# Kernel optimization log

Hardware: AMD Instinct MI355X
Metric: run time of the kernel (lower is better)

## Reference

```python
import jax, jax.numpy as jnp
import numpy as np

IN_DIM = 1024
OUT_DIM = 1024
NUM_EXPERTS = 8
TOP_K = 2
B = 8192


def setup_inputs() -> dict:
    key = jax.random.key(0)
    ks = jax.random.split(key, 8)
    s_in = 1.0 / np.sqrt(IN_DIM)
    s_out = 1.0 / np.sqrt(OUT_DIM)
    return {
        "x": jax.random.normal(ks[0], (B, IN_DIM), dtype=jnp.float32),
        # router Linear(in_dim, num_experts)
        "rw": jax.random.uniform(ks[1], (IN_DIM, NUM_EXPERTS), jnp.float32, -s_in, s_in),
        "rb": jax.random.uniform(ks[2], (NUM_EXPERTS,), jnp.float32, -s_in, s_in),
        # expert MLPs stacked along expert axis
        "w1": jax.random.uniform(ks[3], (NUM_EXPERTS, IN_DIM, OUT_DIM), jnp.float32, -s_in, s_in),
        "b1": jax.random.uniform(ks[4], (NUM_EXPERTS, OUT_DIM), jnp.float32, -s_in, s_in),
        "w2": jax.random.uniform(ks[5], (NUM_EXPERTS, OUT_DIM, OUT_DIM), jnp.float32, -s_out, s_out),
        "b2": jax.random.uniform(ks[6], (NUM_EXPERTS, OUT_DIM), jnp.float32, -s_out, s_out),
    }


def reference(x, rw, rb, w1, b1, w2, b2):
    # ---- TopkRouter ----
    logits = x @ rw + rb                                  # [B, E]
    topk_vals, topk_idx = jax.lax.top_k(logits, TOP_K)    # [B, K]
    neg_inf = jnp.full_like(logits, -jnp.inf)
    rows = jnp.arange(logits.shape[0])[:, None]
    sparse_logits = neg_inf.at[rows, topk_idx].set(topk_vals)
    gating = jax.nn.softmax(sparse_logits, axis=-1)       # zeros outside top-k

    # ---- experts: dense compute, gating weights are exactly 0 for
    # non-selected experts so the weighted combine matches the masked
    # dispatch of the original module. ----
    h = jax.nn.relu(jnp.einsum('bi,eio->beo', x, w1) + b1[None])   # [B, E, out]
    y = jnp.einsum('beh,eho->beo', h, w2) + b2[None]               # [B, E, out]
    fused = jnp.einsum('beo,be->bo', y, gating)                    # [B, out]
    return fused, gating
```

## Files before the change

### kernel.cpp

```cpp
#include <hip/hip_runtime.h>
#include <hip/hip_bf16.h>
#include <cstdint>
#include <cstddef>

#define IN_DIM 1024
#define OUT_DIM 1024
#define NE 8
#define NTOK 8192
#define MT_TILES 20

typedef __bf16 bf16x8 __attribute__((ext_vector_type(8)));
typedef float f32x4 __attribute__((ext_vector_type(4)));
typedef unsigned short ushort8v __attribute__((ext_vector_type(8)));

__device__ __forceinline__ unsigned short f2bf(float f) {
    unsigned u = __float_as_uint(f);
    unsigned r = 0x7fffu + ((u >> 16) & 1u);
    return (unsigned short)((u + r) >> 16);
}

__device__ __forceinline__ void bf2x(unsigned u, float& lo, float& hi) {
    lo = __uint_as_float(u << 16);
    hi = __uint_as_float(u & 0xffff0000u);
}

__device__ __forceinline__ void async16(void* lds, const void* g) {
    __builtin_amdgcn_global_load_lds(
        (const __attribute__((address_space(1))) unsigned int*)g,
        (__attribute__((address_space(3))) unsigned int*)lds,
        16, 0, 0);
}

__global__ __launch_bounds__(256) void convert_transpose_kernel(
    const float* __restrict__ w1, const float* __restrict__ w2,
    unsigned short* __restrict__ w1T, unsigned short* __restrict__ w2T) {
    __shared__ float tile[64][68];
    int z = blockIdx.z;
    const float* src = (z < 8) ? (w1 + (size_t)z * IN_DIM * OUT_DIM)
                               : (w2 + (size_t)(z - 8) * OUT_DIM * OUT_DIM);
    unsigned short* dst = (z < 8) ? (w1T + (size_t)z * IN_DIM * OUT_DIM)
                                  : (w2T + (size_t)(z - 8) * OUT_DIM * OUT_DIM);
    int kt = blockIdx.x * 64, nt = blockIdx.y * 64;
    int t = threadIdx.x;
    int r = t >> 2, cq = (t & 3) * 16;
#pragma unroll
    for (int q = 0; q < 4; ++q) {
        float4 v = *(const float4*)(src + (size_t)(kt + r) * 1024 + nt + cq + q * 4);
        tile[r][cq + q * 4 + 0] = v.x;
        tile[r][cq + q * 4 + 1] = v.y;
        tile[r][cq + q * 4 + 2] = v.z;
        tile[r][cq + q * 4 + 3] = v.w;
    }
    __syncthreads();
    int n = t >> 2, kq = (t & 3) * 16;
#pragma unroll
    for (int q = 0; q < 2; ++q) {
        ushort8v o;
#pragma unroll
        for (int i = 0; i < 8; ++i) o[i] = f2bf(tile[kq + q * 8 + i][n]);
        *(ushort8v*)(dst + (size_t)(nt + n) * 1024 + kt + kq + q * 8) = o;
    }
}

__global__ __launch_bounds__(256) void router_kernel(
    const float* __restrict__ x, const float* __restrict__ rw,
    const float* __restrict__ rb,
    unsigned short* __restrict__ xb,
    float* __restrict__ gating, int* __restrict__ enc,
    float2* __restrict__ gw, int* __restrict__ cnt) {
    __shared__ float srw[NE * IN_DIM];
    int t = threadIdx.x;
    if (blockIdx.x == 0 && t < NE) cnt[t] = 0;
#pragma unroll
    for (int i = 0; i < 4; ++i) {
        int k = t + i * 256;
        float4 a = *(const float4*)(rw + (size_t)k * NE);
        float4 b = *(const float4*)(rw + (size_t)k * NE + 4);
        srw[0 * IN_DIM + k] = a.x; srw[1 * IN_DIM + k] = a.y;
        srw[2 * IN_DIM + k] = a.z; srw[3 * IN_DIM + k] = a.w;
        srw[4 * IN_DIM + k] = b.x; srw[5 * IN_DIM + k] = b.y;
        srw[6 * IN_DIM + k] = b.z; srw[7 * IN_DIM + k] = b.w;
    }
    __syncthreads();
    int wave = t >> 6, lane = t & 63;
    int tok = blockIdx.x * 4 + wave;
    const float* xrow = x + (size_t)tok * IN_DIM;
    unsigned short* xbrow = xb + (size_t)tok * IN_DIM;
    float acc[NE] = {0, 0, 0, 0, 0, 0, 0, 0};
#pragma unroll
    for (int i = 0; i < 4; ++i) {
        int k = i * 256 + lane * 4;
        float4 xv = *(const float4*)(xrow + k);
        ushort4 o;
        o.x = f2bf(xv.x); o.y = f2bf(xv.y); o.z = f2bf(xv.z); o.w = f2bf(xv.w);
        *(ushort4*)(xbrow + k) = o;
#pragma unroll
        for (int e = 0; e < NE; ++e) {
            float4 wv = *(const float4*)(srw + e * IN_DIM + k);
            acc[e] = fmaf(xv.x, wv.x, fmaf(xv.y, wv.y, fmaf(xv.z, wv.z, fmaf(xv.w, wv.w, acc[e]))));
        }
    }
#pragma unroll
    for (int e = 0; e < NE; ++e) {
#pragma unroll
        for (int off = 32; off > 0; off >>= 1) acc[e] += __shfl_xor(acc[e], off);
        acc[e] += rb[e];
    }
    int e0 = 0; float v0 = acc[0];
#pragma unroll
    for (int e = 1; e < NE; ++e) if (acc[e] > v0) { v0 = acc[e]; e0 = e; }
    int e1 = -1; float v1 = -3.4e38f;
#pragma unroll
    for (int e = 0; e < NE; ++e) if (e != e0 && acc[e] > v1) { v1 = acc[e]; e1 = e; }
    float tg = __expf(v1 - v0);
    float inv = 1.0f / (1.0f + tg);
    float g0 = inv, g1 = tg * inv;
    if (lane < NE) gating[(size_t)tok * NE + lane] = (lane == e0) ? g0 : ((lane == e1) ? g1 : 0.0f);
    if (lane == 0) {
        enc[tok] = e0 | (e1 << 8);
        gw[tok] = make_float2(g0, g1);
    }
}

__global__ __launch_bounds__(256) void bucket_kernel(
    const int* __restrict__ enc,
    int* __restrict__ bidx, int* __restrict__ slots, int* __restrict__ cnt) {
    int tok = blockIdx.x * 256 + threadIdx.x;
    int lane = threadIdx.x & 63;
    int v = enc[tok];
    int e0 = v & 0xff, e1 = (v >> 8) & 0xff;
    unsigned long long below = (1ull << lane) - 1ull;
    int p0 = 0, p1 = 0;
#pragma unroll
    for (int e = 0; e < NE; ++e) {
        unsigned long long m0 = __ballot(e0 == e);
        unsigned long long m1 = __ballot(e1 == e);
        int c0 = __popcll(m0), c1 = __popcll(m1);
        int base = 0;
        if (lane == 0 && (c0 + c1)) base = atomicAdd(&cnt[e], c0 + c1);
        base = __shfl(base, 0);
        if (e0 == e) p0 = base + __popcll(m0 & below);
        if (e1 == e) p1 = base + c0 + __popcll(m1 & below);
    }
    bidx[e0 * NTOK + p0] = tok;
    bidx[e1 * NTOK + p1] = tok;
    slots[2 * tok + 0] = (e0 << 13) | p0;
    slots[2 * tok + 1] = (e1 << 13) | p1;
}

__device__ __forceinline__ int prefix_cnt(const int* __restrict__ cnt, int e) {
    int s = 0;
    for (int i = 0; i < NE; ++i) s += (i < e) ? cnt[i] : 0;
    return s;
}

__device__ __forceinline__ void kstep(const unsigned short* Ab,
                                      const unsigned short* Bb,
                                      f32x4 (&acc)[4][4], int wm, int wn,
                                      int lhalf, int slot) {
    bf16x8 av[4], bv[4];
#pragma unroll
    for (int i = 0; i < 4; ++i)
        av[i] = *(const bf16x8*)(Ab + (wm * 32 + i * 8 + lhalf) * 64 + slot);
#pragma unroll
    for (int j = 0; j < 4; ++j)
        bv[j] = *(const bf16x8*)(Bb + (wn * 32 + j * 8 + lhalf) * 64 + slot);
#pragma unroll
    for (int i = 0; i < 4; ++i)
#pragma unroll
        for (int j = 0; j < 4; ++j)
            acc[i][j] = __builtin_amdgcn_mfma_f32_16x16x32_bf16(av[i], bv[j], acc[i][j], 0, 0, 0);
}


__global__ __launch_bounds__(256) void gemm1_kernel(
    const unsigned short* __restrict__ xb, const unsigned short* __restrict__ w1T,
    const float* __restrict__ b1, const int* __restrict__ bidx,
    const int* __restrict__ cnt,
    unsigned short* __restrict__ H) {
    int b = blockIdx.x;
    int e = b & 7;
    int t2 = b >> 3;
    int nt = t2 & 7;
    int mt = t2 >> 3;
    int n_e = cnt[e];
    if (mt * 128 >= n_e) return;
    __shared__ __attribute__((aligned(16))) unsigned short As[3][64 * 64];
    __shared__ __attribute__((aligned(16))) unsigned short Bs[3][64 * 64];
    int t = threadIdx.x, wave = t >> 6, lane = t & 63;
    const int* be = bidx + e * NTOK;
    const unsigned short* agp[2]; const unsigned short* bgp[2];
    int ldsoff[2];
#pragma unroll
    for (int is = 0; is < 2; ++is) {
        int c = is * 256 + t;
        int line = c >> 3;
        int chunkg = (c & 7) ^ (line & 7);
        int sub = chunkg >> 2;
        int growl = 2 * line + sub;
        int growlB = (line >> 5) * 64 + (line & 7) * 8 + sub * 4 + ((line >> 3) & 3);
        int gcol = (chunkg & 3) * 8;
        int gra = mt * 128 + growl;
        int grac = gra < n_e ? gra : n_e - 1;
        agp[is] = xb + (size_t)be[grac] * IN_DIM + gcol;
        bgp[is] = w1T + ((size_t)e * OUT_DIM + nt * 128 + growlB) * IN_DIM + gcol;
        ldsoff[is] = (is * 256 + wave * 64) * 8;
    }
    int wm = wave & 1, wn = wave >> 1;
    int quad = lane >> 4, l15 = lane & 15;
    int lhalf = l15 >> 1;
    int slot = (((l15 & 1) * 4 + quad) ^ lhalf) * 8;
    f32x4 zero4 = {0.f, 0.f, 0.f, 0.f};
    f32x4 acc[4][4];
#pragma unroll
    for (int i = 0; i < 4; ++i)
#pragma unroll
        for (int j = 0; j < 4; ++j) acc[i][j] = zero4;

#pragma unroll
    for (int pt = 0; pt < 2; ++pt)
#pragma unroll
        for (int is = 0; is < 2; ++is) {
            async16(&As[pt][ldsoff[is]], agp[is] + pt * 32);
            async16(&Bs[pt][ldsoff[is]], bgp[is] + pt * 32);
        }
    int cb = 0, sb = 2;
    for (int it = 0; it < 31; ++it) {
        asm volatile("s_waitcnt vmcnt(4)\n\ts_barrier" ::: "memory");
        if (it < 30) {
            int ktn = (it + 2) * 32;
#pragma unroll
            for (int is = 0; is < 2; ++is) {
                async16(&As[sb][ldsoff[is]], agp[is] + ktn);
                async16(&Bs[sb][ldsoff[is]], bgp[is] + ktn);
            }
        }
        kstep(As[cb], Bs[cb], acc, wm, wn, lhalf, slot);
        cb = (cb == 2) ? 0 : cb + 1;
        sb = (sb == 2) ? 0 : sb + 1;
    }
    asm volatile("s_waitcnt vmcnt(0)\n\ts_barrier" ::: "memory");
    kstep(As[cb], Bs[cb], acc, wm, wn, lhalf, slot);

    int hbase = prefix_cnt(cnt, e);
    const float* b1e = b1 + (size_t)e * OUT_DIM;
    int n0 = nt * 128 + wn * 64 + l15 * 4;
    float4 bias = *(const float4*)(b1e + n0);
#pragma unroll
    for (int i = 0; i < 4; ++i) {
        int m0 = mt * 128 + wm * 64 + i * 16 + quad * 4;
#pragma unroll
        for (int r = 0; r < 4; ++r) {
            int gm = m0 + r;
            if (gm < n_e) {
                float h0 = acc[i][0][r] + bias.x; h0 = h0 > 0.f ? h0 : 0.f;
                float h1 = acc[i][1][r] + bias.y; h1 = h1 > 0.f ? h1 : 0.f;
                float h2 = acc[i][2][r] + bias.z; h2 = h2 > 0.f ? h2 : 0.f;
                float h3 = acc[i][3][r] + bias.w; h3 = h3 > 0.f ? h3 : 0.f;
                ushort4 o;
                o.x = f2bf(h0); o.y = f2bf(h1); o.z = f2bf(h2); o.w = f2bf(h3);
                *(ushort4*)(H + (size_t)(hbase + gm) * OUT_DIM + n0) = o;
            }
        }
    }
}

__global__ __launch_bounds__(256) void gemm2_kernel(
    const unsigned short* __restrict__ H, const unsigned short* __restrict__ w2T,
    const int* __restrict__ cnt,
    unsigned short* __restrict__ Y) {
    int b = blockIdx.x;
    int e = b & 7;
    int t2 = b >> 3;
    int nt = t2 & 7;
    int mt = t2 >> 3;
    int n_e = cnt[e];
    if (mt * 128 >= n_e) return;
    __shared__ __attribute__((aligned(16))) unsigned short As[3][64 * 64];
    __shared__ __attribute__((aligned(16))) unsigned short Bs[3][64 * 64];
    int t = threadIdx.x, wave = t >> 6, lane = t & 63;
    int hbase = prefix_cnt(cnt, e);
    const unsigned short* agp[2]; const unsigned short* bgp[2];
    int ldsoff[2];
#pragma unroll
    for (int is = 0; is < 2; ++is) {
        int c = is * 256 + t;
        int line = c >> 3;
        int chunkg = (c & 7) ^ (line & 7);
        int sub = chunkg >> 2;
        int growl = 2 * line + sub;
        int growlB = (line >> 5) * 64 + (line & 7) * 8 + sub * 4 + ((line >> 3) & 3);
        int gcol = (chunkg & 3) * 8;
        int gra = mt * 128 + growl;
        int grac = gra < n_e ? gra : n_e - 1;
        agp[is] = H + (size_t)(hbase + grac) * OUT_DIM + gcol;
        bgp[is] = w2T + ((size_t)e * OUT_DIM + nt * 128 + growlB) * OUT_DIM + gcol;
        ldsoff[is] = (is * 256 + wave * 64) * 8;
    }
    int wm = wave & 1, wn = wave >> 1;
    int quad = lane >> 4, l15 = lane & 15;
    int lhalf = l15 >> 1;
    int slot = (((l15 & 1) * 4 + quad) ^ lhalf) * 8;
    f32x4 zero4 = {0.f, 0.f, 0.f, 0.f};
    f32x4 acc[4][4];
#pragma unroll
    for (int i = 0; i < 4; ++i)
#pragma unroll
        for (int j = 0; j < 4; ++j) acc[i][j] = zero4;

#pragma unroll
    for (int pt = 0; pt < 2; ++pt)
#pragma unroll
        for (int is = 0; is < 2; ++is) {
            async16(&As[pt][ldsoff[is]], agp[is] + pt * 32);
            async16(&Bs[pt][ldsoff[is]], bgp[is] + pt * 32);
        }
    int cb = 0, sb = 2;
    for (int it = 0; it < 31; ++it) {
        asm volatile("s_waitcnt vmcnt(4)\n\ts_barrier" ::: "memory");
        if (it < 30) {
            int ktn = (it + 2) * 32;
#pragma unroll
            for (int is = 0; is < 2; ++is) {
                async16(&As[sb][ldsoff[is]], agp[is] + ktn);
                async16(&Bs[sb][ldsoff[is]], bgp[is] + ktn);
            }
        }
        kstep(As[cb], Bs[cb], acc, wm, wn, lhalf, slot);
        cb = (cb == 2) ? 0 : cb + 1;
        sb = (sb == 2) ? 0 : sb + 1;
    }
    asm volatile("s_waitcnt vmcnt(0)\n\ts_barrier" ::: "memory");
    kstep(As[cb], Bs[cb], acc, wm, wn, lhalf, slot);

    int n0 = nt * 128 + wn * 64 + l15 * 4;
#pragma unroll
    for (int i = 0; i < 4; ++i) {
        int m0 = mt * 128 + wm * 64 + i * 16 + quad * 4;
#pragma unroll
        for (int r = 0; r < 4; ++r) {
            int gm = m0 + r;
            if (gm < n_e) {
                ushort4 o;
                o.x = f2bf(acc[i][0][r]); o.y = f2bf(acc[i][1][r]);
                o.z = f2bf(acc[i][2][r]); o.w = f2bf(acc[i][3][r]);
                *(ushort4*)(Y + (size_t)(hbase + gm) * OUT_DIM + n0) = o;
            }
        }
    }
}

__global__ __launch_bounds__(256) void combine_kernel(
    const unsigned short* __restrict__ Y, const float* __restrict__ b2,
    const float2* __restrict__ gw, const int* __restrict__ slots,
    const int* __restrict__ cnt, float* __restrict__ out) {
    int t = threadIdx.x, wave = t >> 6, lane = t & 63;
    int tok = blockIdx.x * 4 + wave;
    int pre[NE];
    {
        int s = 0;
#pragma unroll
        for (int i = 0; i < NE; ++i) { pre[i] = s; s += cnt[i]; }
    }
    int s0 = slots[2 * tok], s1 = slots[2 * tok + 1];
    int e0 = s0 >> 13, e1 = s1 >> 13;
    int r0 = pre[e0] + (s0 & 8191);
    int r1 = pre[e1] + (s1 & 8191);
    float2 g = gw[tok];
    const unsigned short* y0 = Y + (size_t)r0 * OUT_DIM;
    const unsigned short* y1 = Y + (size_t)r1 * OUT_DIM;
    const float* c0 = b2 + (size_t)e0 * OUT_DIM;
    const float* c1 = b2 + (size_t)e1 * OUT_DIM;
    float* orow = out + (size_t)tok * OUT_DIM;
#pragma unroll
    for (int i = 0; i < 2; ++i) {
        int c = i * 512 + lane * 8;
        uint4 ua = *(const uint4*)(y0 + c);
        uint4 ub = *(const uint4*)(y1 + c);
        float a[8], b[8];
        bf2x(ua.x, a[0], a[1]); bf2x(ua.y, a[2], a[3]);
        bf2x(ua.z, a[4], a[5]); bf2x(ua.w, a[6], a[7]);
        bf2x(ub.x, b[0], b[1]); bf2x(ub.y, b[2], b[3]);
        bf2x(ub.z, b[4], b[5]); bf2x(ub.w, b[6], b[7]);
        float4 p0 = *(const float4*)(c0 + c);
        float4 p1 = *(const float4*)(c0 + c + 4);
        float4 q0 = *(const float4*)(c1 + c);
        float4 q1 = *(const float4*)(c1 + c + 4);
        float o[8];
        o[0] = g.x * (a[0] + p0.x) + g.y * (b[0] + q0.x);
        o[1] = g.x * (a[1] + p0.y) + g.y * (b[1] + q0.y);
        o[2] = g.x * (a[2] + p0.z) + g.y * (b[2] + q0.z);
        o[3] = g.x * (a[3] + p0.w) + g.y * (b[3] + q0.w);
        o[4] = g.x * (a[4] + p1.x) + g.y * (b[4] + q1.x);
        o[5] = g.x * (a[5] + p1.y) + g.y * (b[5] + q1.y);
        o[6] = g.x * (a[6] + p1.z) + g.y * (b[6] + q1.z);
        o[7] = g.x * (a[7] + p1.w) + g.y * (b[7] + q1.w);
        *(float4*)(orow + c) = make_float4(o[0], o[1], o[2], o[3]);
        *(float4*)(orow + c + 4) = make_float4(o[4], o[5], o[6], o[7]);
    }
}

extern "C" void kernel_launch(void* const* d_in, const int* in_sizes, int n_in,
                              void* d_out, int out_size, void* d_ws, size_t ws_size,
                              hipStream_t stream) {
    const float* x  = (const float*)d_in[0];
    const float* rw = (const float*)d_in[1];
    const float* rb = (const float*)d_in[2];
    const float* w1 = (const float*)d_in[3];
    const float* b1 = (const float*)d_in[4];
    const float* w2 = (const float*)d_in[5];
    const float* b2 = (const float*)d_in[6];
    float* out = (float*)d_out;
    float* gating = out + (size_t)NTOK * OUT_DIM;

    char* ws = (char*)d_ws;
    unsigned short* xb  = (unsigned short*)(ws + 0);
    unsigned short* Y   = (unsigned short*)(ws + 0);
    unsigned short* w1T = (unsigned short*)(ws + 16777216);
    unsigned short* w2T = (unsigned short*)(ws + 33554432);
    unsigned short* H   = (unsigned short*)(ws + 50331648);
    int*   bidx  = (int*)(ws + 83886080);
    int*   slots = (int*)(ws + 84148224);
    int*   cnt   = (int*)(ws + 84213760);
    int*    enc  = (int*)(ws + 84213888);
    float2* gw   = (float2*)(ws + 84246656);

    convert_transpose_kernel<<<dim3(16, 16, 16), 256, 0, stream>>>(w1, w2, w1T, w2T);
    router_kernel<<<NTOK / 4, 256, 0, stream>>>(x, rw, rb, xb, gating, enc, gw, cnt);
    bucket_kernel<<<NTOK / 256, 256, 0, stream>>>(enc, bidx, slots, cnt);
    gemm1_kernel<<<8 * 8 * MT_TILES, 256, 0, stream>>>(xb, w1T, b1, bidx, cnt, H);
    gemm2_kernel<<<8 * 8 * MT_TILES, 256, 0, stream>>>(H, w2T, cnt, Y);
    combine_kernel<<<NTOK / 4, 256, 0, stream>>>(Y, b2, gw, slots, cnt, out);
    (void)in_sizes; (void)n_in; (void)out_size; (void)ws_size;
}
```

Before: 294.7 us.

## Enlarge expert GEMM M-tile to 256 rows with 8x4 MFMA accumulators per wave

Doubles the token (M) tile of both expert GEMMs from 128 to 256 rows, so each wave computes 8x4 MFMA blocks instead of 4x4. Each B (weight) tile loaded into LDS is now reused across twice as many rows, cutting weight traffic and halving the grid. The cost is larger A buffers in LDS (triple-buffered), more accumulator registers with a launch-bounds occupancy hint of 2, and coarser tiles that waste more work on ragged per-expert token counts.

```diff
diff --git a/kernel.cpp b/kernel.cpp
--- a/kernel.cpp
+++ b/kernel.cpp
@@ -7,7 +7,7 @@
 #define OUT_DIM 1024
 #define NE 8
 #define NTOK 8192
-#define MT_TILES 20
+#define MT_TILES 10
 
 typedef __bf16 bf16x8 __attribute__((ext_vector_type(8)));
 typedef float f32x4 __attribute__((ext_vector_type(4)));
@@ -156,24 +156,24 @@
 
 __device__ __forceinline__ void kstep(const unsigned short* Ab,
                                       const unsigned short* Bb,
-                                      f32x4 (&acc)[4][4], int wm, int wn,
+                                      f32x4 (&acc)[8][4], int wm, int wn,
                                       int lhalf, int slot) {
-    bf16x8 av[4], bv[4];
-#pragma unroll
-    for (int i = 0; i < 4; ++i)
-        av[i] = *(const bf16x8*)(Ab + (wm * 32 + i * 8 + lhalf) * 64 + slot);
+    bf16x8 av[8], bv[4];
+#pragma unroll
+    for (int i = 0; i < 8; ++i)
+        av[i] = *(const bf16x8*)(Ab + (wm * 64 + i * 8 + lhalf) * 64 + slot);
 #pragma unroll
     for (int j = 0; j < 4; ++j)
         bv[j] = *(const bf16x8*)(Bb + (wn * 32 + j * 8 + lhalf) * 64 + slot);
 #pragma unroll
-    for (int i = 0; i < 4; ++i)
+    for (int i = 0; i < 8; ++i)
 #pragma unroll
         for (int j = 0; j < 4; ++j)
             acc[i][j] = __builtin_amdgcn_mfma_f32_16x16x32_bf16(av[i], bv[j], acc[i][j], 0, 0, 0);
 }
 
 
-__global__ __launch_bounds__(256) void gemm1_kernel(
+__global__ __launch_bounds__(256, 2) void gemm1_kernel(
     const unsigned short* __restrict__ xb, const unsigned short* __restrict__ w1T,
     const float* __restrict__ b1, const int* __restrict__ bidx,
     const int* __restrict__ cnt,
@@ -184,56 +184,64 @@
     int nt = t2 & 7;
     int mt = t2 >> 3;
     int n_e = cnt[e];
-    if (mt * 128 >= n_e) return;
-    __shared__ __attribute__((aligned(16))) unsigned short As[3][64 * 64];
+    if (mt * 256 >= n_e) return;
+    __shared__ __attribute__((aligned(16))) unsigned short As[3][128 * 64];
     __shared__ __attribute__((aligned(16))) unsigned short Bs[3][64 * 64];
     int t = threadIdx.x, wave = t >> 6, lane = t & 63;
     const int* be = bidx + e * NTOK;
-    const unsigned short* agp[2]; const unsigned short* bgp[2];
-    int ldsoff[2];
+    const unsigned short* agp[4]; const unsigned short* bgp[2];
+    int ldsoffA[4], ldsoffB[2];
+#pragma unroll
+    for (int is = 0; is < 4; ++is) {
+        int c = is * 256 + t;
+        int line = c >> 3;
+        int chunkg = (c & 7) ^ (line & 7);
+        int sub = chunkg >> 2;
+        int growl = 2 * line + sub;
+        int gcol = (chunkg & 3) * 8;
+        int gra = mt * 256 + growl;
+        int grac = gra < n_e ? gra : n_e - 1;
+        agp[is] = xb + (size_t)be[grac] * IN_DIM + gcol;
+        ldsoffA[is] = (is * 256 + wave * 64) * 8;
+    }
 #pragma unroll
     for (int is = 0; is < 2; ++is) {
         int c = is * 256 + t;
         int line = c >> 3;
         int chunkg = (c & 7) ^ (line & 7);
         int sub = chunkg >> 2;
-        int growl = 2 * line + sub;
         int growlB = (line >> 5) * 64 + (line & 7) * 8 + sub * 4 + ((line >> 3) & 3);
         int gcol = (chunkg & 3) * 8;
-        int gra = mt * 128 + growl;
-        int grac = gra < n_e ? gra : n_e - 1;
-        agp[is] = xb + (size_t)be[grac] * IN_DIM + gcol;
         bgp[is] = w1T + ((size_t)e * OUT_DIM + nt * 128 + growlB) * IN_DIM + gcol;
-        ldsoff[is] = (is * 256 + wave * 64) * 8;
+        ldsoffB[is] = (is * 256 + wave * 64) * 8;
     }
     int wm = wave & 1, wn = wave >> 1;
     int quad = lane >> 4, l15 = lane & 15;
     int lhalf = l15 >> 1;
     int slot = (((l15 & 1) * 4 + quad) ^ lhalf) * 8;
     f32x4 zero4 = {0.f, 0.f, 0.f, 0.f};
-    f32x4 acc[4][4];
-#pragma unroll
-    for (int i = 0; i < 4; ++i)
+    f32x4 acc[8][4];
+#pragma unroll
+    for (int i = 0; i < 8; ++i)
 #pragma unroll
         for (int j = 0; j < 4; ++j) acc[i][j] = zero4;
 
 #pragma unroll
-    for (int pt = 0; pt < 2; ++pt)
-#pragma unroll
-        for (int is = 0; is < 2; ++is) {
-            async16(&As[pt][ldsoff[is]], agp[is] + pt * 32);
-            async16(&Bs[pt][ldsoff[is]], bgp[is] + pt * 32);
-        }
+    for (int pt = 0; pt < 2; ++pt) {
+#pragma unroll
+        for (int is = 0; is < 4; ++is) async16(&As[pt][ldsoffA[is]], agp[is] + pt * 32);
+#pragma unroll
+        for (int is = 0; is < 2; ++is) async16(&Bs[pt][ldsoffB[is]], bgp[is] + pt * 32);
+    }
     int cb = 0, sb = 2;
     for (int it = 0; it < 31; ++it) {
-        asm volatile("s_waitcnt vmcnt(4)\n\ts_barrier" ::: "memory");
+        asm volatile("s_waitcnt vmcnt(6)\n\ts_barrier" ::: "memory");
         if (it < 30) {
             int ktn = (it + 2) * 32;
 #pragma unroll
-            for (int is = 0; is < 2; ++is) {
-                async16(&As[sb][ldsoff[is]], agp[is] + ktn);
-                async16(&Bs[sb][ldsoff[is]], bgp[is] + ktn);
-            }
+            for (int is = 0; is < 4; ++is) async16(&As[sb][ldsoffA[is]], agp[is] + ktn);
+#pragma unroll
+            for (int is = 0; is < 2; ++is) async16(&Bs[sb][ldsoffB[is]], bgp[is] + ktn);
         }
         kstep(As[cb], Bs[cb], acc, wm, wn, lhalf, slot);
         cb = (cb == 2) ? 0 : cb + 1;
@@ -247,8 +255,8 @@
     int n0 = nt * 128 + wn * 64 + l15 * 4;
     float4 bias = *(const float4*)(b1e + n0);
 #pragma unroll
-    for (int i = 0; i < 4; ++i) {
-        int m0 = mt * 128 + wm * 64 + i * 16 + quad * 4;
+    for (int i = 0; i < 8; ++i) {
+        int m0 = mt * 256 + wm * 128 + i * 16 + quad * 4;
 #pragma unroll
         for (int r = 0; r < 4; ++r) {
             int gm = m0 + r;
@@ -265,7 +273,7 @@
     }
 }
 
-__global__ __launch_bounds__(256) void gemm2_kernel(
+__global__ __launch_bounds__(256, 2) void gemm2_kernel(
     const unsigned short* __restrict__ H, const unsigned short* __restrict__ w2T,
     const int* __restrict__ cnt,
     unsigned short* __restrict__ Y) {
@@ -275,56 +283,64 @@
     int nt = t2 & 7;
     int mt = t2 >> 3;
     int n_e = cnt[e];
-    if (mt * 128 >= n_e) return;
-    __shared__ __attribute__((aligned(16))) unsigned short As[3][64 * 64];
+    if (mt * 256 >= n_e) return;
+    __shared__ __attribute__((aligned(16))) unsigned short As[3][128 * 64];
     __shared__ __attribute__((aligned(16))) unsigned short Bs[3][64 * 64];
     int t = threadIdx.x, wave = t >> 6, lane = t & 63;
     int hbase = prefix_cnt(cnt, e);
-    const unsigned short* agp[2]; const unsigned short* bgp[2];
-    int ldsoff[2];
+    const unsigned short* agp[4]; const unsigned short* bgp[2];
+    int ldsoffA[4], ldsoffB[2];
+#pragma unroll
+    for (int is = 0; is < 4; ++is) {
+        int c = is * 256 + t;
+        int line = c >> 3;
+        int chunkg = (c & 7) ^ (line & 7);
+        int sub = chunkg >> 2;
+        int growl = 2 * line + sub;
+        int gcol = (chunkg & 3) * 8;
+        int gra = mt * 256 + growl;
+        int grac = gra < n_e ? gra : n_e - 1;
+        agp[is] = H + (size_t)(hbase + grac) * OUT_DIM + gcol;
+        ldsoffA[is] = (is * 256 + wave * 64) * 8;
+    }
 #pragma unroll
     for (int is = 0; is < 2; ++is) {
         int c = is * 256 + t;
         int line = c >> 3;
         int chunkg = (c & 7) ^ (line & 7);
         int sub = chunkg >> 2;
-        int growl = 2 * line + sub;
         int growlB = (line >> 5) * 64 + (line & 7) * 8 + sub * 4 + ((line >> 3) & 3);
         int gcol = (chunkg & 3) * 8;
-        int gra = mt * 128 + growl;
-        int grac = gra < n_e ? gra : n_e - 1;
-        agp[is] = H + (size_t)(hbase + grac) * OUT_DIM + gcol;
         bgp[is] = w2T + ((size_t)e * OUT_DIM + nt * 128 + growlB) * OUT_DIM + gcol;
-        ldsoff[is] = (is * 256 + wave * 64) * 8;
+        ldsoffB[is] = (is * 256 + wave * 64) * 8;
     }
     int wm = wave & 1, wn = wave >> 1;
     int quad = lane >> 4, l15 = lane & 15;
     int lhalf = l15 >> 1;
     int slot = (((l15 & 1) * 4 + quad) ^ lhalf) * 8;
     f32x4 zero4 = {0.f, 0.f, 0.f, 0.f};
-    f32x4 acc[4][4];
-#pragma unroll
-    for (int i = 0; i < 4; ++i)
+    f32x4 acc[8][4];
+#pragma unroll
+    for (int i = 0; i < 8; ++i)
 #pragma unroll
         for (int j = 0; j < 4; ++j) acc[i][j] = zero4;
 
 #pragma unroll
-    for (int pt = 0; pt < 2; ++pt)
-#pragma unroll
-        for (int is = 0; is < 2; ++is) {
-            async16(&As[pt][ldsoff[is]], agp[is] + pt * 32);
-            async16(&Bs[pt][ldsoff[is]], bgp[is] + pt * 32);
-        }
+    for (int pt = 0; pt < 2; ++pt) {
+#pragma unroll
+        for (int is = 0; is < 4; ++is) async16(&As[pt][ldsoffA[is]], agp[is] + pt * 32);
+#pragma unroll
+        for (int is = 0; is < 2; ++is) async16(&Bs[pt][ldsoffB[is]], bgp[is] + pt * 32);
+    }
     int cb = 0, sb = 2;
     for (int it = 0; it < 31; ++it) {
-        asm volatile("s_waitcnt vmcnt(4)\n\ts_barrier" ::: "memory");
+        asm volatile("s_waitcnt vmcnt(6)\n\ts_barrier" ::: "memory");
         if (it < 30) {
             int ktn = (it + 2) * 32;
 #pragma unroll
-            for (int is = 0; is < 2; ++is) {
-                async16(&As[sb][ldsoff[is]], agp[is] + ktn);
-                async16(&Bs[sb][ldsoff[is]], bgp[is] + ktn);
-            }
+            for (int is = 0; is < 4; ++is) async16(&As[sb][ldsoffA[is]], agp[is] + ktn);
+#pragma unroll
+            for (int is = 0; is < 2; ++is) async16(&Bs[sb][ldsoffB[is]], bgp[is] + ktn);
         }
         kstep(As[cb], Bs[cb], acc, wm, wn, lhalf, slot);
         cb = (cb == 2) ? 0 : cb + 1;
@@ -335,8 +351,8 @@
 
     int n0 = nt * 128 + wn * 64 + l15 * 4;
 #pragma unroll
-    for (int i = 0; i < 4; ++i) {
-        int m0 = mt * 128 + wm * 64 + i * 16 + quad * 4;
+    for (int i = 0; i < 8; ++i) {
+        int m0 = mt * 256 + wm * 128 + i * 16 + quad * 4;
 #pragma unroll
         for (int r = 0; r < 4; ++r) {
             int gm = m0 + r;
```

Measured after the change: 307.3 us. 1.04x slower.
